# Kernel tuning notes

Hardware: AMD Instinct MI355X
Metric: run time of the kernel (lower is better)

## Reference

```python
import jax, jax.numpy as jnp
import numpy as np

F32 = jnp.float32
G_VEC = jnp.array([0.0, 0.0, -9.80665], dtype=F32)
# KITTI-style filter parameters (process / initial covariances)
COV_OMEGA = 1e-3; COV_ACC = 1e-2; COV_B_OMEGA = 6e-9; COV_B_ACC = 2e-4
COV_ROT_C_I = 1e-9; COV_T_C_I = 1e-9
COV_ROT0 = 1e-3; COV_V0 = 1e-1; COV_B_OMEGA0 = 1e-1; COV_B_ACC0 = 1e-1
COV_ROT_C_I0 = 1e-6; COV_T_C_I0 = 1e-5
Q_DIAG = jnp.array([COV_OMEGA]*3 + [COV_ACC]*3 + [COV_B_OMEGA]*3 + [COV_B_ACC]*3
                   + [COV_ROT_C_I]*3 + [COV_T_C_I]*3, dtype=F32)


def skew(x):
    z = jnp.zeros((), x.dtype)
    return jnp.stack([jnp.stack([z, -x[2], x[1]]),
                      jnp.stack([x[2], z, -x[0]]),
                      jnp.stack([-x[1], x[0], z])])


def so3exp(phi):
    I = jnp.eye(3, dtype=phi.dtype)
    angle = jnp.linalg.norm(phi)
    small = angle < 1e-8
    a = jnp.where(small, 1.0, angle)
    S = skew(phi)
    R = I + (jnp.sin(a) / a) * S + ((1.0 - jnp.cos(a)) / (a * a)) * (S @ S)
    return jnp.where(small, I + S, R)


def sen3exp(xi):
    phi = xi[:3]
    I = jnp.eye(3, dtype=xi.dtype)
    angle = jnp.linalg.norm(phi)
    small = angle < 1e-8
    a = jnp.where(small, 1.0, angle)
    S = skew(phi)
    SS = S @ S
    Rot = jnp.where(small, I + S,
                    I + (jnp.sin(a) / a) * S + ((1.0 - jnp.cos(a)) / (a * a)) * SS)
    J = jnp.where(small, I + 0.5 * S,
                  I + ((1.0 - jnp.cos(a)) / (a * a)) * S + ((a - jnp.sin(a)) / (a ** 3)) * SS)
    x = J @ xi[3:9].reshape(2, 3).T  # (3,2): columns dv, dp
    return Rot, x


def from_rpy(roll, pitch, yaw):
    c, s = jnp.cos, jnp.sin
    z = jnp.zeros((), roll.dtype); o = jnp.ones((), roll.dtype)
    Rz = jnp.stack([jnp.stack([c(yaw), -s(yaw), z]), jnp.stack([s(yaw), c(yaw), z]), jnp.stack([z, z, o])])
    Ry = jnp.stack([jnp.stack([c(pitch), z, s(pitch)]), jnp.stack([z, o, z]), jnp.stack([-s(pitch), z, c(pitch)])])
    Rx = jnp.stack([jnp.stack([o, z, z]), jnp.stack([z, c(roll), -s(roll)]), jnp.stack([z, s(roll), c(roll)])])
    return Rz @ Ry @ Rx


def _run(t, u, measurements_covs, v_mes, ang0, w_init):
    I3 = jnp.eye(3, dtype=F32)
    IdP = jnp.eye(21, dtype=F32)
    Q = jnp.diag(Q_DIAG)
    dt = t[1:] - t[:-1]
    # InitProcessCovNet.init_cov: beta = 10 ** tanh(W @ 1)
    beta = 10.0 ** jnp.tanh(w_init)
    P0 = jnp.zeros((21, 21), F32)
    I2 = jnp.eye(2, dtype=F32)
    P0 = P0.at[:2, :2].set(COV_ROT0 * beta[0] * I2)
    P0 = P0.at[3:5, 3:5].set(COV_V0 * beta[1] * I2)
    P0 = P0.at[9:12, 9:12].set(COV_B_OMEGA0 * beta[2] * I3)
    P0 = P0.at[12:15, 12:15].set(COV_B_ACC0 * beta[3] * I3)
    P0 = P0.at[15:18, 15:18].set(COV_ROT_C_I0 * beta[4] * I3)
    P0 = P0.at[18:21, 18:21].set(COV_T_C_I0 * beta[5] * I3)
    Rot0 = from_rpy(ang0[0], ang0[1], ang0[2])
    z3 = jnp.zeros(3, F32)
    state0 = (Rot0, v_mes[0], z3, z3, z3, I3, z3, P0)

    def step(carry, inp):
        Rot_p, v_p, p_p, bo_p, ba_p, Rci_p, tci_p, P = carry
        u_i, dt_i, mc_i = inp
        # ---- propagate ----
        acc = Rot_p @ (u_i[3:6] - ba_p) + G_VEC
        v = v_p + acc * dt_i
        p = p_p + v_p * dt_i + 0.5 * acc * dt_i * dt_i
        omega = (u_i[:3] - bo_p) * dt_i
        Rot = Rot_p @ so3exp(omega)
        # ---- covariance propagation ----
        vsr = skew(v_p) @ Rot_p
        psr = skew(p_p) @ Rot_p
        F = jnp.zeros((21, 21), F32)
        F = F.at[3:6, :3].set(skew(G_VEC))
        F = F.at[6:9, 3:6].set(I3)
        F = F.at[3:6, 12:15].set(-Rot_p)
        F = F.at[:3, 9:12].set(-Rot_p)
        F = F.at[3:6, 9:12].set(-vsr)
        F = F.at[6:9, 9:12].set(-psr)
        Gm = jnp.zeros((21, 18), F32)
        Gm = Gm.at[:3, :3].set(Rot_p)
        Gm = Gm.at[3:6, 3:6].set(Rot_p)
        Gm = Gm.at[3:6, :3].set(vsr)
        Gm = Gm.at[6:9, :3].set(psr)
        Gm = Gm.at[9:12, 6:9].set(I3)
        Gm = Gm.at[12:15, 9:12].set(I3)
        Gm = Gm.at[15:18, 12:15].set(I3)
        Gm = Gm.at[18:21, 15:18].set(I3)
        F = F * dt_i
        Gm = Gm * dt_i
        F2 = F @ F
        Phi = IdP + F + 0.5 * F2 + (F2 @ F) / 6.0
        P = Phi @ (P + Gm @ Q @ Gm.T) @ Phi.T
        # ---- update (zero lateral/vertical body velocity pseudo-measurement) ----
        Rot_body = Rot @ Rci_p
        v_imu = Rot.T @ v
        om = u_i[:3] - bo_p
        v_body = Rci_p.T @ v_imu + skew(tci_p) @ om
        Omega = skew(om)
        H_v_imu = Rci_p.T @ skew(v_imu)
        H_t = skew(tci_p)
        H = jnp.zeros((2, 21), F32)
        H = H.at[:, 3:6].set(Rot_body.T[1:])
        H = H.at[:, 15:18].set(H_v_imu[1:])
        H = H.at[:, 9:12].set(H_t[1:])
        H = H.at[:, 18:21].set(-Omega[1:])
        r = -v_body[1:]
        Rm = jnp.diag(mc_i)
        S = H @ P @ H.T + Rm
        K = jnp.linalg.solve(S, (P @ H.T).T).T  # (21,2)
        dx = K @ r
        dR, dxi = sen3exp(dx[:9])
        Rot_u = dR @ Rot
        v_u = dR @ v + dxi[:, 0]
        p_u = dR @ p + dxi[:, 1]
        bo_u = bo_p + dx[9:12]
        ba_u = ba_p + dx[12:15]
        Rci_u = so3exp(dx[15:18]) @ Rci_p
        tci_u = tci_p + dx[18:21]
        I_KH = IdP - K @ H
        P_u = I_KH @ P @ I_KH.T + K @ Rm @ K.T
        P_u = 0.5 * (P_u + P_u.T)
        new = (Rot_u, v_u, p_u, bo_u, ba_u, Rci_u, tci_u, P_u)
        return new, (Rot_u, v_u, p_u, bo_u, ba_u, Rci_u, tci_u)

    xs = (u[1:], dt, measurements_covs[1:])
    _, traj = jax.lax.scan(step, state0, xs)
    cat = lambda x0, xs_: jnp.concatenate([x0[None], xs_], axis=0)
    Rot = cat(Rot0, traj[0]); v = cat(state0[1], traj[1]); p = cat(state0[2], traj[2])
    bo = cat(state0[3], traj[3]); ba = cat(state0[4], traj[4])
    Rci = cat(I3, traj[5]); tci = cat(state0[6], traj[6])
    n = Rot.shape[0]
    # pack (Rot, v, p, b_omega, b_acc, Rot_c_i, t_c_i) -> [N, 30]
    return jnp.concatenate([Rot.reshape(n, 9), v, p, bo, ba, Rci.reshape(n, 9), tci], axis=1)


def setup_inputs() -> dict:
    key = jax.random.key(0)
    k1, k2, k3, k4, k5, k6 = jax.random.split(key, 6)
    N = 5000
    t = jnp.arange(N, dtype=F32) * 0.01  # 100 Hz IMU timestamps
    u = 0.1 * jax.random.normal(k1, (N, 6), dtype=F32)
    u = u.at[:, 5].add(9.80665)  # accel z ~ gravity
    measurements_covs = 0.5 * jax.random.uniform(k2, (N, 2), dtype=F32) + 0.1
    v_mes = jax.random.normal(k3, (N, 3), dtype=F32)
    p_mes = jax.random.normal(k4, (N, 3), dtype=F32)
    ang0 = 0.1 * jax.random.normal(k5, (3,), dtype=F32)
    w_init = 0.1 * jax.random.normal(k6, (6,), dtype=F32)
    return {"t": t, "u": u, "measurements_covs": measurements_covs,
            "v_mes": v_mes, "p_mes": p_mes, "ang0": ang0, "w_init": w_init, "N": N}


def reference(t, u, measurements_covs, v_mes, p_mes, ang0, w_init, N):
    # p_mes is accepted (as in run()) but unused: p[0] stays zero in init_run.
    return _run(t, u, measurements_covs, v_mes, ang0, w_init)
```

## Files before the change

kernel.cpp:

```cpp
#include <hip/hip_runtime.h>
#include <math.h>

#define GRV 9.80665f

__device__ __forceinline__ void so3coeffs(float a2, float* c1, float* c2, float* c3){
  if (a2 < 2.5e-3f){
    float a4 = a2*a2;
    *c1 = 1.f      - a2*(1.f/6.f)   + a4*(1.f/120.f);
    *c2 = 0.5f     - a2*(1.f/24.f)  + a4*(1.f/720.f);
    *c3 = (1.f/6.f)- a2*(1.f/120.f) + a4*(1.f/5040.f);
  } else {
    float a = sqrtf(a2);
    float sa = sinf(a), ca = cosf(a);
    *c1 = sa/a; *c2 = (1.f-ca)/a2; *c3 = (a-sa)/(a2*a);
  }
}

__device__ __forceinline__ void so3exp_u(float p0, float p1, float p2, float* R){
  float a2 = p0*p0+p1*p1+p2*p2;
  float c1,c2,c3; so3coeffs(a2,&c1,&c2,&c3);
  R[0]=1.f+c2*(p0*p0-a2); R[4]=1.f+c2*(p1*p1-a2); R[8]=1.f+c2*(p2*p2-a2);
  R[1]=-c1*p2+c2*p0*p1;   R[3]= c1*p2+c2*p0*p1;
  R[2]= c1*p1+c2*p0*p2;   R[6]=-c1*p1+c2*p0*p2;
  R[5]=-c1*p0+c2*p1*p2;   R[7]= c1*p0+c2*p1*p2;
}

__device__ __forceinline__ void mat3mul_u(const float* A, const float* B, float* C){
  #pragma unroll
  for (int r=0;r<3;r++)
    #pragma unroll
    for (int c=0;c<3;c++)
      C[r*3+c] = A[r*3]*B[c] + A[r*3+1]*B[3+c] + A[r*3+2]*B[6+c];
}

__device__ __forceinline__ void col_update(float* a, const float* R_, const float* n13,
                                           const float* n23, float dtv, float hdt2,
                                           float Gdt, float Ghdt2){
  float nb[9];
  #pragma unroll
  for (int jb=0;jb<3;jb++)
    nb[jb] = a[jb] - dtv*(R_[jb*3]*a[9]+R_[jb*3+1]*a[10]+R_[jb*3+2]*a[11]);
  #pragma unroll
  for (int r=0;r<3;r++){
    float s = a[3+r];
    if (r==0) s += Gdt*a[1];
    if (r==1) s -= Gdt*a[0];
    s += n13[r*3]*a[9]+n13[r*3+1]*a[10]+n13[r*3+2]*a[11];
    s -= dtv*(R_[r*3]*a[12]+R_[r*3+1]*a[13]+R_[r*3+2]*a[14]);
    nb[3+r]=s;
  }
  #pragma unroll
  for (int r=0;r<3;r++){
    float s = a[6+r];
    if (r==0) s += Ghdt2*a[1];
    if (r==1) s -= Ghdt2*a[0];
    s += dtv*a[3+r];
    s += n23[r*3]*a[9]+n23[r*3+1]*a[10]+n23[r*3+2]*a[11];
    s -= hdt2*(R_[r*3]*a[12]+R_[r*3+1]*a[13]+R_[r*3+2]*a[14]);
    nb[6+r]=s;
  }
  #pragma unroll
  for (int k=0;k<9;k++) a[k]=nb[k];
}

__global__ __launch_bounds__(64)
void iekf_kernel(const float* __restrict__ t, const float* __restrict__ u,
                 const float* __restrict__ mcov, const float* __restrict__ vmes,
                 const float* __restrict__ ang0, const float* __restrict__ winit,
                 float* __restrict__ out, int N)
{
  const int lane = threadIdx.x;
  const int cl   = (lane<21)? lane : 20;

  __shared__ float TP1[21*24];
  __shared__ float TP2[21*24];
  __shared__ float PH[44];
  __shared__ float stG[36];

  float R_[9], v_[3], p_[3], bo_[3], ba_[3], Rci_[9], tci_[3];
  float creg[21];

  float beta[6];
  #pragma unroll
  for (int k=0;k<6;k++) beta[k] = powf(10.f, tanhf(winit[k]));
  {
    float cr=cosf(ang0[0]), sr=sinf(ang0[0]);
    float cp=cosf(ang0[1]), sp=sinf(ang0[1]);
    float cy=cosf(ang0[2]), sy=sinf(ang0[2]);
    float Rz[9]={cy,-sy,0.f, sy,cy,0.f, 0.f,0.f,1.f};
    float Ry[9]={cp,0.f,sp, 0.f,1.f,0.f, -sp,0.f,cp};
    float Rx[9]={1.f,0.f,0.f, 0.f,cr,-sr, 0.f,sr,cr};
    float T1m[9]; mat3mul_u(Rz,Ry,T1m); mat3mul_u(T1m,Rx,R_);
  }
  v_[0]=vmes[0]; v_[1]=vmes[1]; v_[2]=vmes[2];
  #pragma unroll
  for (int k=0;k<3;k++){ p_[k]=0.f; bo_[k]=0.f; ba_[k]=0.f; tci_[k]=0.f; }
  #pragma unroll
  for (int k=0;k<9;k++) Rci_[k] = (k%4==0)?1.f:0.f;

  {
    float dl = (lane==0||lane==1)? 1e-3f*beta[0]
             : (lane==3||lane==4)? 0.1f*beta[1]
             : (lane>=9&&lane<12)? 0.1f*beta[2]
             : (lane>=12&&lane<15)? 0.1f*beta[3]
             : (lane>=15&&lane<18)? 1e-6f*beta[4]
             : (lane>=18&&lane<21)? 1e-5f*beta[5] : 0.f;
    #pragma unroll
    for (int j=0;j<21;j++) creg[j] = (j==lane)? dl : 0.f;
  }

  if (lane==0){
    ((float4*)stG)[0] = make_float4(R_[0],R_[1],R_[2],R_[3]);
    ((float4*)stG)[1] = make_float4(R_[4],R_[5],R_[6],R_[7]);
    ((float4*)stG)[2] = make_float4(R_[8],v_[0],v_[1],v_[2]);
    ((float4*)stG)[3] = make_float4(p_[0],p_[1],p_[2],bo_[0]);
    ((float4*)stG)[4] = make_float4(bo_[1],bo_[2],ba_[0],ba_[1]);
    ((float4*)stG)[5] = make_float4(ba_[2],Rci_[0],Rci_[1],Rci_[2]);
    ((float4*)stG)[6] = make_float4(Rci_[3],Rci_[4],Rci_[5],Rci_[6]);
    ((float4*)stG)[7] = make_float4(Rci_[7],Rci_[8],tci_[0],tci_[1]);
    ((float4*)stG)[8] = make_float4(tci_[2],0.f,0.f,0.f);
  }

  float t_nm1 = t[0];
  float t_n   = (N>1)? t[1] : t[0];
  float mc0   = (N>1)? mcov[2] : 0.f;
  float mc1   = (N>1)? mcov[3] : 0.f;
  float u6[6] = {0,0,0,0,0,0};
  if (N>1){
    #pragma unroll
    for (int k=0;k<6;k++) u6[k]=u[6+k];
  }

  for (int n=1; n<N; n++){
    const float dtv = t_n - t_nm1;
    const float dt2 = dtv*dtv;
    const float hdt2 = 0.5f*dt2;
    const float sdt3 = dt2*dtv*(1.f/6.f);
    const float Gdt = GRV*dtv;
    const float Ghdt2 = GRV*hdt2;

    if (lane<33) out[(size_t)(n-1)*33 + lane] = stG[lane];

    if (lane<21){
      float4* rp = (float4*)&TP1[lane*24];
      rp[0]=make_float4(creg[0],creg[1],creg[2],creg[3]);
      rp[1]=make_float4(creg[4],creg[5],creg[6],creg[7]);
      rp[2]=make_float4(creg[8],creg[9],creg[10],creg[11]);
      rp[3]=make_float4(creg[12],creg[13],creg[14],creg[15]);
      rp[4]=make_float4(creg[16],creg[17],creg[18],creg[19]);
      TP1[lane*24+20]=creg[20];
    }
    float colv[21];
    #pragma unroll
    for (int r=0;r<21;r++) colv[r] = TP1[r*24+cl];

    float vsr[9], psr[9], n13[9], n23[9];
    #pragma unroll
    for (int c=0;c<3;c++){
      vsr[c]   = v_[1]*R_[6+c] - v_[2]*R_[3+c];
      vsr[3+c] = v_[2]*R_[c]   - v_[0]*R_[6+c];
      vsr[6+c] = v_[0]*R_[3+c] - v_[1]*R_[c];
      psr[c]   = p_[1]*R_[6+c] - p_[2]*R_[3+c];
      psr[3+c] = p_[2]*R_[c]   - p_[0]*R_[6+c];
      psr[6+c] = p_[0]*R_[3+c] - p_[1]*R_[c];
    }
    #pragma unroll
    for (int c=0;c<3;c++){
      float sg0 =  GRV*R_[3+c];
      float sg1 = -GRV*R_[c];
      n13[c]   = -dtv*vsr[c]   - hdt2*sg0;
      n13[3+c] = -dtv*vsr[3+c] - hdt2*sg1;
      n13[6+c] = -dtv*vsr[6+c];
      n23[c]   = -dtv*psr[c]   - hdt2*vsr[c]   - sdt3*sg0;
      n23[3+c] = -dtv*psr[3+c] - hdt2*vsr[3+c] - sdt3*sg1;
      n23[6+c] = -dtv*psr[6+c] - hdt2*vsr[6+c];
    }
    const float vv = v_[0]*v_[0]+v_[1]*v_[1]+v_[2]*v_[2];
    const float vp = v_[0]*p_[0]+v_[1]*p_[1]+v_[2]*p_[2];
    const float pp = p_[0]*p_[0]+p_[1]*p_[1]+p_[2]*p_[2];

    float areg[21];
    #pragma unroll
    for (int j=0;j<21;j++) areg[j] = 0.5f*(creg[j] + colv[j]);
    {
      const float qom = 1e-3f*dt2, qac = 1e-2f*dt2;
      if (lane<9){
        int bi = lane/3, r3 = lane - 3*bi;
        float vrr = (r3==0)?v_[0]:(r3==1)?v_[1]:v_[2];
        float prr = (r3==0)?p_[0]:(r3==1)?p_[1]:p_[2];
        float sv0 = (r3==0)?0.f:(r3==1)? v_[2]:-v_[1];
        float sv1 = (r3==0)?-v_[2]:(r3==1)?0.f: v_[0];
        float sv2 = (r3==0)? v_[1]:(r3==1)?-v_[0]:0.f;
        float sp0 = (r3==0)?0.f:(r3==1)? p_[2]:-p_[1];
        float sp1 = (r3==0)?-p_[2]:(r3==1)?0.f: p_[0];
        float sp2 = (r3==0)? p_[1]:(r3==1)?-p_[0]:0.f;
        if (bi==0){
          areg[r3]  += qom;
          areg[3] -= qom*sv0; areg[4] -= qom*sv1; areg[5] -= qom*sv2;
          areg[6] -= qom*sp0; areg[7] -= qom*sp1; areg[8] -= qom*sp2;
        } else if (bi==1){
          areg[0] += qom*sv0; areg[1] += qom*sv1; areg[2] += qom*sv2;
          areg[3+r3] += qom*vv + qac;
          areg[3] -= qom*vrr*v_[0]; areg[4] -= qom*vrr*v_[1]; areg[5] -= qom*vrr*v_[2];
          areg[6+r3] += qom*vp;
          areg[6] -= qom*prr*v_[0]; areg[7] -= qom*prr*v_[1]; areg[8] -= qom*prr*v_[2];
        } else {
          areg[0] += qom*sp0; areg[1] += qom*sp1; areg[2] += qom*sp2;
          areg[3+r3] += qom*vp;
          areg[3] -= qom*vrr*p_[0]; areg[4] -= qom*vrr*p_[1]; areg[5] -= qom*vrr*p_[2];
          areg[6+r3] += qom*pp;
          areg[6] -= qom*prr*p_[0]; areg[7] -= qom*prr*p_[1]; areg[8] -= qom*prr*p_[2];
        }
      }
      #pragma unroll
      for (int j=9;j<21;j++){
        float qd = (j<12)? 6e-9f : (j<15)? 2e-4f : 1e-9f;
        areg[j] += (lane==j)? qd*dt2 : 0.f;
      }
    }

    col_update(areg, R_, n13, n23, dtv, hdt2, Gdt, Ghdt2);

    if (lane<21){
      float4* rp = (float4*)&TP2[lane*24];
      rp[0]=make_float4(areg[0],areg[1],areg[2],areg[3]);
      rp[1]=make_float4(areg[4],areg[5],areg[6],areg[7]);
      rp[2]=make_float4(areg[8],areg[9],areg[10],areg[11]);
      rp[3]=make_float4(areg[12],areg[13],areg[14],areg[15]);
      rp[4]=make_float4(areg[16],areg[17],areg[18],areg[19]);
      TP2[lane*24+20]=areg[20];
    }
    float ctreg[21];
    #pragma unroll
    for (int r=0;r<21;r++) ctreg[r] = TP2[r*24+cl];

    float Rn[9], vnp[3], pnp[3];
    {
      float ub0=u6[3]-ba_[0], ub1=u6[4]-ba_[1], ub2=u6[5]-ba_[2];
      float ac0=R_[0]*ub0+R_[1]*ub1+R_[2]*ub2;
      float ac1=R_[3]*ub0+R_[4]*ub1+R_[5]*ub2;
      float ac2=R_[6]*ub0+R_[7]*ub1+R_[8]*ub2 - GRV;
      vnp[0]=v_[0]+ac0*dtv; vnp[1]=v_[1]+ac1*dtv; vnp[2]=v_[2]+ac2*dtv;
      pnp[0]=p_[0]+v_[0]*dtv+0.5f*ac0*dt2;
      pnp[1]=p_[1]+v_[1]*dtv+0.5f*ac1*dt2;
      pnp[2]=p_[2]+v_[2]*dtv+0.5f*ac2*dt2;
      float E[9]; so3exp_u((u6[0]-bo_[0])*dtv,(u6[1]-bo_[1])*dtv,(u6[2]-bo_[2])*dtv, E);
      mat3mul_u(R_, E, Rn);
    }
    float h0_3,h0_4,h0_5,h0_9,h0_11,h0_15,h0_16,h0_17,h0_18,h0_20;
    float h1_3,h1_4,h1_5,h1_9,h1_10,h1_15,h1_16,h1_17,h1_18,h1_19;
    float rsh0, rsh1;
    {
      float Rb[9]; mat3mul_u(Rn, Rci_, Rb);
      float vi0 = Rn[0]*vnp[0]+Rn[3]*vnp[1]+Rn[6]*vnp[2];
      float vi1 = Rn[1]*vnp[0]+Rn[4]*vnp[1]+Rn[7]*vnp[2];
      float vi2 = Rn[2]*vnp[0]+Rn[5]*vnp[1]+Rn[8]*vnp[2];
      float o0 = u6[0]-bo_[0], o1 = u6[1]-bo_[1], o2 = u6[2]-bo_[2];
      h0_3 = Rb[1]; h0_4 = Rb[4]; h0_5 = Rb[7];
      h1_3 = Rb[2]; h1_4 = Rb[5]; h1_5 = Rb[8];
      h0_9 = tci_[2];  h0_11 = -tci_[0];
      h1_9 = -tci_[1]; h1_10 = tci_[0];
      h0_15 =  Rci_[4]*vi2 - Rci_[7]*vi1;
      h0_16 = -Rci_[1]*vi2 + Rci_[7]*vi0;
      h0_17 =  Rci_[1]*vi1 - Rci_[4]*vi0;
      h1_15 =  Rci_[5]*vi2 - Rci_[8]*vi1;
      h1_16 = -Rci_[2]*vi2 + Rci_[8]*vi0;
      h1_17 =  Rci_[2]*vi1 - Rci_[5]*vi0;
      h0_18 = -o2; h0_20 = o0;
      h1_18 =  o1; h1_19 = -o0;
      rsh0 = -( Rci_[1]*vi0 + Rci_[4]*vi1 + Rci_[7]*vi2 + (tci_[2]*o0 - tci_[0]*o2) );
      rsh1 = -( Rci_[2]*vi0 + Rci_[5]*vi1 + Rci_[8]*vi2 + (-tci_[1]*o0 + tci_[0]*o1) );
    }

    col_update(ctreg, R_, n13, n23, dtv, hdt2, Gdt, Ghdt2);

    float ph0 = (((ctreg[3]*h0_3 + ctreg[4]*h0_4) + (ctreg[5]*h0_5 + ctreg[9]*h0_9)) +
                 ((ctreg[11]*h0_11 + ctreg[15]*h0_15) + (ctreg[16]*h0_16 + ctreg[17]*h0_17))) +
                (ctreg[18]*h0_18 + ctreg[20]*h0_20);
    float ph1 = (((ctreg[3]*h1_3 + ctreg[4]*h1_4) + (ctreg[5]*h1_5 + ctreg[9]*h1_9)) +
                 ((ctreg[10]*h1_10 + ctreg[15]*h1_15) + (ctreg[16]*h1_16 + ctreg[17]*h1_17))) +
                (ctreg[18]*h1_18 + ctreg[19]*h1_19);
    if (lane<21) *(float2*)&PH[lane*2] = make_float2(ph0, ph1);

    float pj0[21], pj1[21];
    {
      #pragma unroll
      for (int q=0;q<11;q++){
        float4 v4 = ((float4*)PH)[q];
        if (2*q   < 21){ pj0[2*q]   = v4.x; pj1[2*q]   = v4.y; }
        if (2*q+1 < 21){ pj0[2*q+1] = v4.z; pj1[2*q+1] = v4.w; }
      }
    }

    float s00 = mc0 + ((((h0_3*pj0[3] + h0_4*pj0[4]) + (h0_5*pj0[5] + h0_9*pj0[9])) +
                        ((h0_11*pj0[11] + h0_15*pj0[15]) + (h0_16*pj0[16] + h0_17*pj0[17]))) +
                       (h0_18*pj0[18] + h0_20*pj0[20]));
    float s01 =        ((((h0_3*pj1[3] + h0_4*pj1[4]) + (h0_5*pj1[5] + h0_9*pj1[9])) +
                        ((h0_11*pj1[11] + h0_15*pj1[15]) + (h0_16*pj1[16] + h0_17*pj1[17]))) +
                       (h0_18*pj1[18] + h0_20*pj1[20]));
    float s10 =        ((((h1_3*pj0[3] + h1_4*pj0[4]) + (h1_5*pj0[5] + h1_9*pj0[9])) +
                        ((h1_10*pj0[10] + h1_15*pj0[15]) + (h1_16*pj0[16] + h1_17*pj0[17]))) +
                       (h1_18*pj0[18] + h1_19*pj0[19]));
    float s11 = mc1 + ((((h1_3*pj1[3] + h1_4*pj1[4]) + (h1_5*pj1[5] + h1_9*pj1[9])) +
                        ((h1_10*pj1[10] + h1_15*pj1[15]) + (h1_16*pj1[16] + h1_17*pj1[17]))) +
                       (h1_18*pj1[18] + h1_19*pj1[19]));
    float id  = 1.f/(s00*s11 - s01*s10);
    float i00 =  s11*id, i01 = -s01*id, i10 = -s10*id, i11 = s00*id;
    float sm01 = 0.5f*(s01+s10);
    float g0 = i00*rsh0 + i01*rsh1;
    float g1 = i10*rsh0 + i11*rsh1;

    float dx[21];
    #pragma unroll
    for (int j=0;j<21;j++) dx[j] = pj0[j]*g0 + pj1[j]*g1;

    {
      float ki0 = ph0*i00 + ph1*i10;
      float ki1 = ph0*i01 + ph1*i11;
      float ai0 = s00*ki0 + sm01*ki1;
      float ai1 = sm01*ki0 + s11*ki1;
      float al = -ki0 + (ai0 - ph0)*i00 + (ai1 - ph1)*i01;
      float be = -ki1 + (ai0 - ph0)*i10 + (ai1 - ph1)*i11;
      #pragma unroll
      for (int j=0;j<21;j++) creg[j] = ctreg[j] + al*pj0[j] + be*pj1[j];
    }

    {
      float q0=dx[0], q1=dx[1], q2=dx[2];
      float a2 = q0*q0+q1*q1+q2*q2;
      float c1,c2,c3; so3coeffs(a2,&c1,&c2,&c3);
      float dR[9], Jm[9];
      dR[0]=1.f+c2*(q0*q0-a2); dR[4]=1.f+c2*(q1*q1-a2); dR[8]=1.f+c2*(q2*q2-a2);
      dR[1]=-c1*q2+c2*q0*q1;   dR[3]= c1*q2+c2*q0*q1;
      dR[2]= c1*q1+c2*q0*q2;   dR[6]=-c1*q1+c2*q0*q2;
      dR[5]=-c1*q0+c2*q1*q2;   dR[7]= c1*q0+c2*q1*q2;
      Jm[0]=1.f+c3*(q0*q0-a2); Jm[4]=1.f+c3*(q1*q1-a2); Jm[8]=1.f+c3*(q2*q2-a2);
      Jm[1]=-c2*q2+c3*q0*q1;   Jm[3]= c2*q2+c3*q0*q1;
      Jm[2]= c2*q1+c3*q0*q2;   Jm[6]=-c2*q1+c3*q0*q2;
      Jm[5]=-c2*q0+c3*q1*q2;   Jm[7]= c2*q0+c3*q1*q2;
      float xv[3], xp[3];
      #pragma unroll
      for (int r=0;r<3;r++){
        xv[r]=Jm[r*3]*dx[3]+Jm[r*3+1]*dx[4]+Jm[r*3+2]*dx[5];
        xp[r]=Jm[r*3]*dx[6]+Jm[r*3+1]*dx[7]+Jm[r*3+2]*dx[8];
      }
      float Rn2[9]; mat3mul_u(dR, Rn, Rn2);
      #pragma unroll
      for (int r=0;r<3;r++){
        float vv2 = dR[r*3]*vnp[0]+dR[r*3+1]*vnp[1]+dR[r*3+2]*vnp[2] + xv[r];
        float pp2 = dR[r*3]*pnp[0]+dR[r*3+1]*pnp[1]+dR[r*3+2]*pnp[2] + xp[r];
        v_[r]=vv2; p_[r]=pp2;
        bo_[r]+=dx[9+r]; ba_[r]+=dx[12+r]; tci_[r]+=dx[18+r];
      }
      float E2[9]; so3exp_u(dx[15],dx[16],dx[17],E2);
      float Rc2[9]; mat3mul_u(E2, Rci_, Rc2);
      #pragma unroll
      for (int k=0;k<9;k++){ Rci_[k]=Rc2[k]; R_[k]=Rn2[k]; }
    }
    if (lane==0){
      ((float4*)stG)[0] = make_float4(R_[0],R_[1],R_[2],R_[3]);
      ((float4*)stG)[1] = make_float4(R_[4],R_[5],R_[6],R_[7]);
      ((float4*)stG)[2] = make_float4(R_[8],v_[0],v_[1],v_[2]);
      ((float4*)stG)[3] = make_float4(p_[0],p_[1],p_[2],bo_[0]);
      ((float4*)stG)[4] = make_float4(bo_[1],bo_[2],ba_[0],ba_[1]);
      ((float4*)stG)[5] = make_float4(ba_[2],Rci_[0],Rci_[1],Rci_[2]);
      ((float4*)stG)[6] = make_float4(Rci_[3],Rci_[4],Rci_[5],Rci_[6]);
      ((float4*)stG)[7] = make_float4(Rci_[7],Rci_[8],tci_[0],tci_[1]);
      ((float4*)stG)[8] = make_float4(tci_[2],0.f,0.f,0.f);
    }

    {
      int np = n+1;
      t_nm1 = t_n;
      if (np < N){
        t_n = t[np];
        mc0 = mcov[np*2]; mc1 = mcov[np*2+1];
        #pragma unroll
        for (int k=0;k<6;k++) u6[k]=u[np*6+k];
      }
    }
  }

  if (lane<33) out[(size_t)(N-1)*33 + lane] = stG[lane];
}

extern "C" void kernel_launch(void* const* d_in, const int* in_sizes, int n_in,
                              void* d_out, int out_size, void* d_ws, size_t ws_size,
                              hipStream_t stream) {
  const float* t     = (const float*)d_in[0];
  const float* u     = (const float*)d_in[1];
  const float* mcov  = (const float*)d_in[2];
  const float* vmes  = (const float*)d_in[3];
  const float* ang0  = (const float*)d_in[5];
  const float* winit = (const float*)d_in[6];
  float* out = (float*)d_out;
  int N = in_sizes[0];
  iekf_kernel<<<dim3(1), dim3(64), 0, stream>>>(t, u, mcov, vmes, ang0, winit, out, N);
}
```

Measured before the change: 15.94 ms.

## Split IEKF step across two wavefronts for covariance and state paths

Launches 128 threads and gives the covariance propagation (the two col_update passes and transposes) to wave 0, while wave 1 does state propagation, the measurement Jacobian, the state correction and the output stores. Values pass between the waves through shared memory (state, H, PH), with three block barriers per step. The aim is to run the independent state and covariance work at the same time on one CU instead of serially in a single wave. In exchange it adds barrier and LDS round-trip latency to every step of a strictly sequential loop.

```diff
diff --git a/kernel.cpp b/kernel.cpp
--- a/kernel.cpp
+++ b/kernel.cpp
@@ -63,26 +63,23 @@
   for (int k=0;k<9;k++) a[k]=nb[k];
 }
 
-__global__ __launch_bounds__(64)
+__global__ __launch_bounds__(128)
 void iekf_kernel(const float* __restrict__ t, const float* __restrict__ u,
                  const float* __restrict__ mcov, const float* __restrict__ vmes,
                  const float* __restrict__ ang0, const float* __restrict__ winit,
                  float* __restrict__ out, int N)
 {
-  const int lane = threadIdx.x;
-  const int cl   = (lane<21)? lane : 20;
-
-  __shared__ float TP1[21*24];
-  __shared__ float TP2[21*24];
-  __shared__ float PH[44];
-  __shared__ float stG[36];
+  const int tid  = threadIdx.x;
+  const int lane = tid & 63;
+  const bool w0  = (tid < 64);
+
+  __shared__ float TP[21*24];
+  __shared__ float stS[36];
+  __shared__ float Hb[20];
+  __shared__ float PHb[44];
 
   float R_[9], v_[3], p_[3], bo_[3], ba_[3], Rci_[9], tci_[3];
-  float creg[21];
-
-  float beta[6];
-  #pragma unroll
-  for (int k=0;k<6;k++) beta[k] = powf(10.f, tanhf(winit[k]));
+
   {
     float cr=cosf(ang0[0]), sr=sinf(ang0[0]);
     float cp=cosf(ang0[1]), sp=sinf(ang0[1]);
@@ -98,7 +95,25 @@
   #pragma unroll
   for (int k=0;k<9;k++) Rci_[k] = (k%4==0)?1.f:0.f;
 
-  {
+  if (tid==0){
+    ((float4*)stS)[0] = make_float4(R_[0],R_[1],R_[2],R_[3]);
+    ((float4*)stS)[1] = make_float4(R_[4],R_[5],R_[6],R_[7]);
+    ((float4*)stS)[2] = make_float4(R_[8],v_[0],v_[1],v_[2]);
+    ((float4*)stS)[3] = make_float4(p_[0],p_[1],p_[2],bo_[0]);
+    ((float4*)stS)[4] = make_float4(bo_[1],bo_[2],ba_[0],ba_[1]);
+    ((float4*)stS)[5] = make_float4(ba_[2],Rci_[0],Rci_[1],Rci_[2]);
+    ((float4*)stS)[6] = make_float4(Rci_[3],Rci_[4],Rci_[5],Rci_[6]);
+    ((float4*)stS)[7] = make_float4(Rci_[7],Rci_[8],tci_[0],tci_[1]);
+    ((float4*)stS)[8] = make_float4(tci_[2],0.f,0.f,0.f);
+  }
+
+  float creg[21], colv[21];
+  #pragma unroll
+  for (int j=0;j<21;j++){ creg[j]=0.f; colv[j]=0.f; }
+  if (w0){
+    float beta[6];
+    #pragma unroll
+    for (int k=0;k<6;k++) beta[k] = powf(10.f, tanhf(winit[k]));
     float dl = (lane==0||lane==1)? 1e-3f*beta[0]
              : (lane==3||lane==4)? 0.1f*beta[1]
              : (lane>=9&&lane<12)? 0.1f*beta[2]
@@ -107,18 +122,14 @@
              : (lane>=18&&lane<21)? 1e-5f*beta[5] : 0.f;
     #pragma unroll
     for (int j=0;j<21;j++) creg[j] = (j==lane)? dl : 0.f;
-  }
-
-  if (lane==0){
-    ((float4*)stG)[0] = make_float4(R_[0],R_[1],R_[2],R_[3]);
-    ((float4*)stG)[1] = make_float4(R_[4],R_[5],R_[6],R_[7]);
-    ((float4*)stG)[2] = make_float4(R_[8],v_[0],v_[1],v_[2]);
-    ((float4*)stG)[3] = make_float4(p_[0],p_[1],p_[2],bo_[0]);
-    ((float4*)stG)[4] = make_float4(bo_[1],bo_[2],ba_[0],ba_[1]);
-    ((float4*)stG)[5] = make_float4(ba_[2],Rci_[0],Rci_[1],Rci_[2]);
-    ((float4*)stG)[6] = make_float4(Rci_[3],Rci_[4],Rci_[5],Rci_[6]);
-    ((float4*)stG)[7] = make_float4(Rci_[7],Rci_[8],tci_[0],tci_[1]);
-    ((float4*)stG)[8] = make_float4(tci_[2],0.f,0.f,0.f);
+    if (lane<21){
+      #pragma unroll
+      for (int j=0;j<21;j++) TP[j*24+lane]=creg[j];
+    }
+    if (lane<21){
+      #pragma unroll
+      for (int j=0;j<21;j++) colv[j]=TP[lane*24+j];
+    }
   }
 
   float t_nm1 = t[0];
@@ -126,195 +137,209 @@
   float mc0   = (N>1)? mcov[2] : 0.f;
   float mc1   = (N>1)? mcov[3] : 0.f;
   float u6[6] = {0,0,0,0,0,0};
-  if (N>1){
+  if (!w0 && N>1){
     #pragma unroll
     for (int k=0;k<6;k++) u6[k]=u[6+k];
   }
 
+  __syncthreads();
+
+  float h03=0,h04=0,h05=0,h09=0,h011=0,h015=0,h016=0,h017=0,h018=0,h020=0;
+  float h13=0,h14=0,h15=0,h19=0,h110=0,h115=0,h116=0,h117=0,h118=0,h119=0;
+  float rsh0=0, rsh1=0;
+  float Rn[9], vnp[3], pnp[3];
+  float ctreg[21];
+  float ph0=0.f, ph1=0.f;
+
   for (int n=1; n<N; n++){
-    const float dtv = t_n - t_nm1;
-    const float dt2 = dtv*dtv;
+    const float dtv  = t_n - t_nm1;
+    const float dt2  = dtv*dtv;
     const float hdt2 = 0.5f*dt2;
     const float sdt3 = dt2*dtv*(1.f/6.f);
-    const float Gdt = GRV*dtv;
-    const float Ghdt2 = GRV*hdt2;
-
-    if (lane<33) out[(size_t)(n-1)*33 + lane] = stG[lane];
-
-    if (lane<21){
-      float4* rp = (float4*)&TP1[lane*24];
-      rp[0]=make_float4(creg[0],creg[1],creg[2],creg[3]);
-      rp[1]=make_float4(creg[4],creg[5],creg[6],creg[7]);
-      rp[2]=make_float4(creg[8],creg[9],creg[10],creg[11]);
-      rp[3]=make_float4(creg[12],creg[13],creg[14],creg[15]);
-      rp[4]=make_float4(creg[16],creg[17],creg[18],creg[19]);
-      TP1[lane*24+20]=creg[20];
-    }
-    float colv[21];
-    #pragma unroll
-    for (int r=0;r<21;r++) colv[r] = TP1[r*24+cl];
-
-    float vsr[9], psr[9], n13[9], n23[9];
-    #pragma unroll
-    for (int c=0;c<3;c++){
-      vsr[c]   = v_[1]*R_[6+c] - v_[2]*R_[3+c];
-      vsr[3+c] = v_[2]*R_[c]   - v_[0]*R_[6+c];
-      vsr[6+c] = v_[0]*R_[3+c] - v_[1]*R_[c];
-      psr[c]   = p_[1]*R_[6+c] - p_[2]*R_[3+c];
-      psr[3+c] = p_[2]*R_[c]   - p_[0]*R_[6+c];
-      psr[6+c] = p_[0]*R_[3+c] - p_[1]*R_[c];
-    }
-    #pragma unroll
-    for (int c=0;c<3;c++){
-      float sg0 =  GRV*R_[3+c];
-      float sg1 = -GRV*R_[c];
-      n13[c]   = -dtv*vsr[c]   - hdt2*sg0;
-      n13[3+c] = -dtv*vsr[3+c] - hdt2*sg1;
-      n13[6+c] = -dtv*vsr[6+c];
-      n23[c]   = -dtv*psr[c]   - hdt2*vsr[c]   - sdt3*sg0;
-      n23[3+c] = -dtv*psr[3+c] - hdt2*vsr[3+c] - sdt3*sg1;
-      n23[6+c] = -dtv*psr[6+c] - hdt2*vsr[6+c];
-    }
-    const float vv = v_[0]*v_[0]+v_[1]*v_[1]+v_[2]*v_[2];
-    const float vp = v_[0]*p_[0]+v_[1]*p_[1]+v_[2]*p_[2];
-    const float pp = p_[0]*p_[0]+p_[1]*p_[1]+p_[2]*p_[2];
-
-    float areg[21];
-    #pragma unroll
-    for (int j=0;j<21;j++) areg[j] = 0.5f*(creg[j] + colv[j]);
-    {
-      const float qom = 1e-3f*dt2, qac = 1e-2f*dt2;
-      if (lane<9){
-        int bi = lane/3, r3 = lane - 3*bi;
-        float vrr = (r3==0)?v_[0]:(r3==1)?v_[1]:v_[2];
-        float prr = (r3==0)?p_[0]:(r3==1)?p_[1]:p_[2];
-        float sv0 = (r3==0)?0.f:(r3==1)? v_[2]:-v_[1];
-        float sv1 = (r3==0)?-v_[2]:(r3==1)?0.f: v_[0];
-        float sv2 = (r3==0)? v_[1]:(r3==1)?-v_[0]:0.f;
-        float sp0 = (r3==0)?0.f:(r3==1)? p_[2]:-p_[1];
-        float sp1 = (r3==0)?-p_[2]:(r3==1)?0.f: p_[0];
-        float sp2 = (r3==0)? p_[1]:(r3==1)?-p_[0]:0.f;
-        if (bi==0){
-          areg[r3]  += qom;
-          areg[3] -= qom*sv0; areg[4] -= qom*sv1; areg[5] -= qom*sv2;
-          areg[6] -= qom*sp0; areg[7] -= qom*sp1; areg[8] -= qom*sp2;
-        } else if (bi==1){
-          areg[0] += qom*sv0; areg[1] += qom*sv1; areg[2] += qom*sv2;
-          areg[3+r3] += qom*vv + qac;
-          areg[3] -= qom*vrr*v_[0]; areg[4] -= qom*vrr*v_[1]; areg[5] -= qom*vrr*v_[2];
-          areg[6+r3] += qom*vp;
-          areg[6] -= qom*prr*v_[0]; areg[7] -= qom*prr*v_[1]; areg[8] -= qom*prr*v_[2];
-        } else {
-          areg[0] += qom*sp0; areg[1] += qom*sp1; areg[2] += qom*sp2;
-          areg[3+r3] += qom*vp;
-          areg[3] -= qom*vrr*p_[0]; areg[4] -= qom*vrr*p_[1]; areg[5] -= qom*vrr*p_[2];
-          areg[6+r3] += qom*pp;
-          areg[6] -= qom*prr*p_[0]; areg[7] -= qom*prr*p_[1]; areg[8] -= qom*prr*p_[2];
+    const float Gdt  = GRV*dtv;
+    const float Ghdt2= GRV*hdt2;
+
+    if (w0){
+      {
+        float4 s0=((float4*)stS)[0], s1=((float4*)stS)[1], s2=((float4*)stS)[2], s3=((float4*)stS)[3];
+        R_[0]=s0.x; R_[1]=s0.y; R_[2]=s0.z; R_[3]=s0.w;
+        R_[4]=s1.x; R_[5]=s1.y; R_[6]=s1.z; R_[7]=s1.w;
+        R_[8]=s2.x; v_[0]=s2.y; v_[1]=s2.z; v_[2]=s2.w;
+        p_[0]=s3.x; p_[1]=s3.y; p_[2]=s3.z;
+      }
+      float vsr[9], psr[9], n13[9], n23[9];
+      #pragma unroll
+      for (int c=0;c<3;c++){
+        vsr[c]   = v_[1]*R_[6+c] - v_[2]*R_[3+c];
+        vsr[3+c] = v_[2]*R_[c]   - v_[0]*R_[6+c];
+        vsr[6+c] = v_[0]*R_[3+c] - v_[1]*R_[c];
+        psr[c]   = p_[1]*R_[6+c] - p_[2]*R_[3+c];
+        psr[3+c] = p_[2]*R_[c]   - p_[0]*R_[6+c];
+        psr[6+c] = p_[0]*R_[3+c] - p_[1]*R_[c];
+      }
+      #pragma unroll
+      for (int c=0;c<3;c++){
+        float sg0 =  GRV*R_[3+c];
+        float sg1 = -GRV*R_[c];
+        n13[c]   = -dtv*vsr[c]   - hdt2*sg0;
+        n13[3+c] = -dtv*vsr[3+c] - hdt2*sg1;
+        n13[6+c] = -dtv*vsr[6+c];
+        n23[c]   = -dtv*psr[c]   - hdt2*vsr[c]   - sdt3*sg0;
+        n23[3+c] = -dtv*psr[3+c] - hdt2*vsr[3+c] - sdt3*sg1;
+        n23[6+c] = -dtv*psr[6+c] - hdt2*vsr[6+c];
+      }
+      const float vv = v_[0]*v_[0]+v_[1]*v_[1]+v_[2]*v_[2];
+      const float vp = v_[0]*p_[0]+v_[1]*p_[1]+v_[2]*p_[2];
+      const float pp = p_[0]*p_[0]+p_[1]*p_[1]+p_[2]*p_[2];
+
+      float areg[21];
+      #pragma unroll
+      for (int j=0;j<21;j++) areg[j] = 0.5f*(creg[j] + colv[j]);
+      {
+        const float qom = 1e-3f*dt2, qac = 1e-2f*dt2;
+        if (lane<9){
+          int bi = lane/3, r3 = lane - 3*bi;
+          float vrr = (r3==0)?v_[0]:(r3==1)?v_[1]:v_[2];
+          float prr = (r3==0)?p_[0]:(r3==1)?p_[1]:p_[2];
+          float sv0 = (r3==0)?0.f:(r3==1)? v_[2]:-v_[1];
+          float sv1 = (r3==0)?-v_[2]:(r3==1)?0.f: v_[0];
+          float sv2 = (r3==0)? v_[1]:(r3==1)?-v_[0]:0.f;
+          float sp0 = (r3==0)?0.f:(r3==1)? p_[2]:-p_[1];
+          float sp1 = (r3==0)?-p_[2]:(r3==1)?0.f: p_[0];
+          float sp2 = (r3==0)? p_[1]:(r3==1)?-p_[0]:0.f;
+          if (bi==0){
+            areg[r3]  += qom;
+            areg[3] -= qom*sv0; areg[4] -= qom*sv1; areg[5] -= qom*sv2;
+            areg[6] -= qom*sp0; areg[7] -= qom*sp1; areg[8] -= qom*sp2;
+          } else if (bi==1){
+            areg[0] += qom*sv0; areg[1] += qom*sv1; areg[2] += qom*sv2;
+            areg[3+r3] += qom*vv + qac;
+            areg[3] -= qom*vrr*v_[0]; areg[4] -= qom*vrr*v_[1]; areg[5] -= qom*vrr*v_[2];
+            areg[6+r3] += qom*vp;
+            areg[6] -= qom*prr*v_[0]; areg[7] -= qom*prr*v_[1]; areg[8] -= qom*prr*v_[2];
+          } else {
+            areg[0] += qom*sp0; areg[1] += qom*sp1; areg[2] += qom*sp2;
+            areg[3+r3] += qom*vp;
+            areg[3] -= qom*vrr*p_[0]; areg[4] -= qom*vrr*p_[1]; areg[5] -= qom*vrr*p_[2];
+            areg[6+r3] += qom*pp;
+            areg[6] -= qom*prr*p_[0]; areg[7] -= qom*prr*p_[1]; areg[8] -= qom*prr*p_[2];
+          }
         }
-      }
-      #pragma unroll
-      for (int j=9;j<21;j++){
-        float qd = (j<12)? 6e-9f : (j<15)? 2e-4f : 1e-9f;
-        areg[j] += (lane==j)? qd*dt2 : 0.f;
-      }
-    }
-
-    col_update(areg, R_, n13, n23, dtv, hdt2, Gdt, Ghdt2);
-
-    if (lane<21){
-      float4* rp = (float4*)&TP2[lane*24];
-      rp[0]=make_float4(areg[0],areg[1],areg[2],areg[3]);
-      rp[1]=make_float4(areg[4],areg[5],areg[6],areg[7]);
-      rp[2]=make_float4(areg[8],areg[9],areg[10],areg[11]);
-      rp[3]=make_float4(areg[12],areg[13],areg[14],areg[15]);
-      rp[4]=make_float4(areg[16],areg[17],areg[18],areg[19]);
-      TP2[lane*24+20]=areg[20];
-    }
-    float ctreg[21];
-    #pragma unroll
-    for (int r=0;r<21;r++) ctreg[r] = TP2[r*24+cl];
-
-    float Rn[9], vnp[3], pnp[3];
-    {
-      float ub0=u6[3]-ba_[0], ub1=u6[4]-ba_[1], ub2=u6[5]-ba_[2];
-      float ac0=R_[0]*ub0+R_[1]*ub1+R_[2]*ub2;
-      float ac1=R_[3]*ub0+R_[4]*ub1+R_[5]*ub2;
-      float ac2=R_[6]*ub0+R_[7]*ub1+R_[8]*ub2 - GRV;
-      vnp[0]=v_[0]+ac0*dtv; vnp[1]=v_[1]+ac1*dtv; vnp[2]=v_[2]+ac2*dtv;
-      pnp[0]=p_[0]+v_[0]*dtv+0.5f*ac0*dt2;
-      pnp[1]=p_[1]+v_[1]*dtv+0.5f*ac1*dt2;
-      pnp[2]=p_[2]+v_[2]*dtv+0.5f*ac2*dt2;
-      float E[9]; so3exp_u((u6[0]-bo_[0])*dtv,(u6[1]-bo_[1])*dtv,(u6[2]-bo_[2])*dtv, E);
-      mat3mul_u(R_, E, Rn);
-    }
-    float h0_3,h0_4,h0_5,h0_9,h0_11,h0_15,h0_16,h0_17,h0_18,h0_20;
-    float h1_3,h1_4,h1_5,h1_9,h1_10,h1_15,h1_16,h1_17,h1_18,h1_19;
-    float rsh0, rsh1;
-    {
-      float Rb[9]; mat3mul_u(Rn, Rci_, Rb);
-      float vi0 = Rn[0]*vnp[0]+Rn[3]*vnp[1]+Rn[6]*vnp[2];
-      float vi1 = Rn[1]*vnp[0]+Rn[4]*vnp[1]+Rn[7]*vnp[2];
-      float vi2 = Rn[2]*vnp[0]+Rn[5]*vnp[1]+Rn[8]*vnp[2];
-      float o0 = u6[0]-bo_[0], o1 = u6[1]-bo_[1], o2 = u6[2]-bo_[2];
-      h0_3 = Rb[1]; h0_4 = Rb[4]; h0_5 = Rb[7];
-      h1_3 = Rb[2]; h1_4 = Rb[5]; h1_5 = Rb[8];
-      h0_9 = tci_[2];  h0_11 = -tci_[0];
-      h1_9 = -tci_[1]; h1_10 = tci_[0];
-      h0_15 =  Rci_[4]*vi2 - Rci_[7]*vi1;
-      h0_16 = -Rci_[1]*vi2 + Rci_[7]*vi0;
-      h0_17 =  Rci_[1]*vi1 - Rci_[4]*vi0;
-      h1_15 =  Rci_[5]*vi2 - Rci_[8]*vi1;
-      h1_16 = -Rci_[2]*vi2 + Rci_[8]*vi0;
-      h1_17 =  Rci_[2]*vi1 - Rci_[5]*vi0;
-      h0_18 = -o2; h0_20 = o0;
-      h1_18 =  o1; h1_19 = -o0;
-      rsh0 = -( Rci_[1]*vi0 + Rci_[4]*vi1 + Rci_[7]*vi2 + (tci_[2]*o0 - tci_[0]*o2) );
-      rsh1 = -( Rci_[2]*vi0 + Rci_[5]*vi1 + Rci_[8]*vi2 + (-tci_[1]*o0 + tci_[0]*o1) );
-    }
-
-    col_update(ctreg, R_, n13, n23, dtv, hdt2, Gdt, Ghdt2);
-
-    float ph0 = (((ctreg[3]*h0_3 + ctreg[4]*h0_4) + (ctreg[5]*h0_5 + ctreg[9]*h0_9)) +
-                 ((ctreg[11]*h0_11 + ctreg[15]*h0_15) + (ctreg[16]*h0_16 + ctreg[17]*h0_17))) +
-                (ctreg[18]*h0_18 + ctreg[20]*h0_20);
-    float ph1 = (((ctreg[3]*h1_3 + ctreg[4]*h1_4) + (ctreg[5]*h1_5 + ctreg[9]*h1_9)) +
-                 ((ctreg[10]*h1_10 + ctreg[15]*h1_15) + (ctreg[16]*h1_16 + ctreg[17]*h1_17))) +
-                (ctreg[18]*h1_18 + ctreg[19]*h1_19);
-    if (lane<21) *(float2*)&PH[lane*2] = make_float2(ph0, ph1);
+        #pragma unroll
+        for (int j=9;j<21;j++){
+          float qd = (j<12)? 6e-9f : (j<15)? 2e-4f : 1e-9f;
+          areg[j] += (lane==j)? qd*dt2 : 0.f;
+        }
+      }
+      if (lane>=21){
+        #pragma unroll
+        for (int j=0;j<21;j++) areg[j]=0.f;
+      }
+
+      col_update(areg, R_, n13, n23, dtv, hdt2, Gdt, Ghdt2);
+
+      if (lane<21){
+        #pragma unroll
+        for (int j=0;j<21;j++) TP[j*24+lane]=areg[j];
+      }
+      if (lane<21){
+        #pragma unroll
+        for (int j=0;j<21;j++) ctreg[j]=TP[lane*24+j];
+      } else {
+        #pragma unroll
+        for (int j=0;j<21;j++) ctreg[j]=0.f;
+      }
+
+      col_update(ctreg, R_, n13, n23, dtv, hdt2, Gdt, Ghdt2);
+    } else {
+      if (lane<33) out[(size_t)(n-1)*33 + lane] = stS[lane];
+      {
+        float ub0=u6[3]-ba_[0], ub1=u6[4]-ba_[1], ub2=u6[5]-ba_[2];
+        float ac0=R_[0]*ub0+R_[1]*ub1+R_[2]*ub2;
+        float ac1=R_[3]*ub0+R_[4]*ub1+R_[5]*ub2;
+        float ac2=R_[6]*ub0+R_[7]*ub1+R_[8]*ub2 - GRV;
+        vnp[0]=v_[0]+ac0*dtv; vnp[1]=v_[1]+ac1*dtv; vnp[2]=v_[2]+ac2*dtv;
+        pnp[0]=p_[0]+v_[0]*dtv+0.5f*ac0*dt2;
+        pnp[1]=p_[1]+v_[1]*dtv+0.5f*ac1*dt2;
+        pnp[2]=p_[2]+v_[2]*dtv+0.5f*ac2*dt2;
+        float E[9]; so3exp_u((u6[0]-bo_[0])*dtv,(u6[1]-bo_[1])*dtv,(u6[2]-bo_[2])*dtv, E);
+        mat3mul_u(R_, E, Rn);
+      }
+      {
+        float Rb[9]; mat3mul_u(Rn, Rci_, Rb);
+        float vi0 = Rn[0]*vnp[0]+Rn[3]*vnp[1]+Rn[6]*vnp[2];
+        float vi1 = Rn[1]*vnp[0]+Rn[4]*vnp[1]+Rn[7]*vnp[2];
+        float vi2 = Rn[2]*vnp[0]+Rn[5]*vnp[1]+Rn[8]*vnp[2];
+        float o0 = u6[0]-bo_[0], o1 = u6[1]-bo_[1], o2 = u6[2]-bo_[2];
+        h03 = Rb[1]; h04 = Rb[4]; h05 = Rb[7];
+        h13 = Rb[2]; h14 = Rb[5]; h15 = Rb[8];
+        h09 = tci_[2];  h011 = -tci_[0];
+        h19 = -tci_[1]; h110 = tci_[0];
+        h015 =  Rci_[4]*vi2 - Rci_[7]*vi1;
+        h016 = -Rci_[1]*vi2 + Rci_[7]*vi0;
+        h017 =  Rci_[1]*vi1 - Rci_[4]*vi0;
+        h115 =  Rci_[5]*vi2 - Rci_[8]*vi1;
+        h116 = -Rci_[2]*vi2 + Rci_[8]*vi0;
+        h117 =  Rci_[2]*vi1 - Rci_[5]*vi0;
+        h018 = -o2; h020 = o0;
+        h118 =  o1; h119 = -o0;
+        rsh0 = -( Rci_[1]*vi0 + Rci_[4]*vi1 + Rci_[7]*vi2 + (tci_[2]*o0 - tci_[0]*o2) );
+        rsh1 = -( Rci_[2]*vi0 + Rci_[5]*vi1 + Rci_[8]*vi2 + (-tci_[1]*o0 + tci_[0]*o1) );
+      }
+      if (lane==0){
+        ((float4*)Hb)[0] = make_float4(h03,h04,h05,h09);
+        ((float4*)Hb)[1] = make_float4(h011,h015,h016,h017);
+        ((float4*)Hb)[2] = make_float4(h018,h020,h13,h14);
+        ((float4*)Hb)[3] = make_float4(h15,h19,h110,h115);
+        ((float4*)Hb)[4] = make_float4(h116,h117,h118,h119);
+      }
+    }
+    __syncthreads();
+
+    if (w0){
+      float4 b0=((float4*)Hb)[0], b1=((float4*)Hb)[1], b2=((float4*)Hb)[2];
+      float4 b3=((float4*)Hb)[3], b4=((float4*)Hb)[4];
+      h03=b0.x; h04=b0.y; h05=b0.z; h09=b0.w;
+      h011=b1.x; h015=b1.y; h016=b1.z; h017=b1.w;
+      h018=b2.x; h020=b2.y; h13=b2.z; h14=b2.w;
+      h15=b3.x; h19=b3.y; h110=b3.z; h115=b3.w;
+      h116=b4.x; h117=b4.y; h118=b4.z; h119=b4.w;
+      ph0 = (((ctreg[3]*h03 + ctreg[4]*h04) + (ctreg[5]*h05 + ctreg[9]*h09)) +
+             ((ctreg[11]*h011 + ctreg[15]*h015) + (ctreg[16]*h016 + ctreg[17]*h017))) +
+            (ctreg[18]*h018 + ctreg[20]*h020);
+      ph1 = (((ctreg[3]*h13 + ctreg[4]*h14) + (ctreg[5]*h15 + ctreg[9]*h19)) +
+             ((ctreg[10]*h110 + ctreg[15]*h115) + (ctreg[16]*h116 + ctreg[17]*h117))) +
+            (ctreg[18]*h118 + ctreg[19]*h119);
+      if (lane<21) *(float2*)&PHb[lane*2] = make_float2(ph0, ph1);
+    }
+    __syncthreads();
 
     float pj0[21], pj1[21];
     {
       #pragma unroll
       for (int q=0;q<11;q++){
-        float4 v4 = ((float4*)PH)[q];
+        float4 v4 = ((float4*)PHb)[q];
         if (2*q   < 21){ pj0[2*q]   = v4.x; pj1[2*q]   = v4.y; }
         if (2*q+1 < 21){ pj0[2*q+1] = v4.z; pj1[2*q+1] = v4.w; }
       }
     }
-
-    float s00 = mc0 + ((((h0_3*pj0[3] + h0_4*pj0[4]) + (h0_5*pj0[5] + h0_9*pj0[9])) +
-                        ((h0_11*pj0[11] + h0_15*pj0[15]) + (h0_16*pj0[16] + h0_17*pj0[17]))) +
-                       (h0_18*pj0[18] + h0_20*pj0[20]));
-    float s01 =        ((((h0_3*pj1[3] + h0_4*pj1[4]) + (h0_5*pj1[5] + h0_9*pj1[9])) +
-                        ((h0_11*pj1[11] + h0_15*pj1[15]) + (h0_16*pj1[16] + h0_17*pj1[17]))) +
-                       (h0_18*pj1[18] + h0_20*pj1[20]));
-    float s10 =        ((((h1_3*pj0[3] + h1_4*pj0[4]) + (h1_5*pj0[5] + h1_9*pj0[9])) +
-                        ((h1_10*pj0[10] + h1_15*pj0[15]) + (h1_16*pj0[16] + h1_17*pj0[17]))) +
-                       (h1_18*pj0[18] + h1_19*pj0[19]));
-    float s11 = mc1 + ((((h1_3*pj1[3] + h1_4*pj1[4]) + (h1_5*pj1[5] + h1_9*pj1[9])) +
-                        ((h1_10*pj1[10] + h1_15*pj1[15]) + (h1_16*pj1[16] + h1_17*pj1[17]))) +
-                       (h1_18*pj1[18] + h1_19*pj1[19]));
+    float s00 = mc0 + ((((h03*pj0[3] + h04*pj0[4]) + (h05*pj0[5] + h09*pj0[9])) +
+                        ((h011*pj0[11] + h015*pj0[15]) + (h016*pj0[16] + h017*pj0[17]))) +
+                       (h018*pj0[18] + h020*pj0[20]));
+    float s01 =        ((((h03*pj1[3] + h04*pj1[4]) + (h05*pj1[5] + h09*pj1[9])) +
+                        ((h011*pj1[11] + h015*pj1[15]) + (h016*pj1[16] + h017*pj1[17]))) +
+                       (h018*pj1[18] + h020*pj1[20]));
+    float s10 =        ((((h13*pj0[3] + h14*pj0[4]) + (h15*pj0[5] + h19*pj0[9])) +
+                        ((h110*pj0[10] + h115*pj0[15]) + (h116*pj0[16] + h117*pj0[17]))) +
+                       (h118*pj0[18] + h119*pj0[19]));
+    float s11 = mc1 + ((((h13*pj1[3] + h14*pj1[4]) + (h15*pj1[5] + h19*pj1[9])) +
+                        ((h110*pj1[10] + h115*pj1[15]) + (h116*pj1[16] + h117*pj1[17]))) +
+                       (h118*pj1[18] + h119*pj1[19]));
     float id  = 1.f/(s00*s11 - s01*s10);
     float i00 =  s11*id, i01 = -s01*id, i10 = -s10*id, i11 = s00*id;
     float sm01 = 0.5f*(s01+s10);
-    float g0 = i00*rsh0 + i01*rsh1;
-    float g1 = i10*rsh0 + i11*rsh1;
-
-    float dx[21];
-    #pragma unroll
-    for (int j=0;j<21;j++) dx[j] = pj0[j]*g0 + pj1[j]*g1;
-
-    {
+
+    if (w0){
       float ki0 = ph0*i00 + ph1*i10;
       float ki1 = ph0*i01 + ph1*i11;
       float ai0 = s00*ki0 + sm01*ki1;
@@ -323,50 +348,63 @@
       float be = -ki1 + (ai0 - ph0)*i10 + (ai1 - ph1)*i11;
       #pragma unroll
       for (int j=0;j<21;j++) creg[j] = ctreg[j] + al*pj0[j] + be*pj1[j];
-    }
-
-    {
-      float q0=dx[0], q1=dx[1], q2=dx[2];
-      float a2 = q0*q0+q1*q1+q2*q2;
-      float c1,c2,c3; so3coeffs(a2,&c1,&c2,&c3);
-      float dR[9], Jm[9];
-      dR[0]=1.f+c2*(q0*q0-a2); dR[4]=1.f+c2*(q1*q1-a2); dR[8]=1.f+c2*(q2*q2-a2);
-      dR[1]=-c1*q2+c2*q0*q1;   dR[3]= c1*q2+c2*q0*q1;
-      dR[2]= c1*q1+c2*q0*q2;   dR[6]=-c1*q1+c2*q0*q2;
-      dR[5]=-c1*q0+c2*q1*q2;   dR[7]= c1*q0+c2*q1*q2;
-      Jm[0]=1.f+c3*(q0*q0-a2); Jm[4]=1.f+c3*(q1*q1-a2); Jm[8]=1.f+c3*(q2*q2-a2);
-      Jm[1]=-c2*q2+c3*q0*q1;   Jm[3]= c2*q2+c3*q0*q1;
-      Jm[2]= c2*q1+c3*q0*q2;   Jm[6]=-c2*q1+c3*q0*q2;
-      Jm[5]=-c2*q0+c3*q1*q2;   Jm[7]= c2*q0+c3*q1*q2;
-      float xv[3], xp[3];
-      #pragma unroll
-      for (int r=0;r<3;r++){
-        xv[r]=Jm[r*3]*dx[3]+Jm[r*3+1]*dx[4]+Jm[r*3+2]*dx[5];
-        xp[r]=Jm[r*3]*dx[6]+Jm[r*3+1]*dx[7]+Jm[r*3+2]*dx[8];
-      }
-      float Rn2[9]; mat3mul_u(dR, Rn, Rn2);
-      #pragma unroll
-      for (int r=0;r<3;r++){
-        float vv2 = dR[r*3]*vnp[0]+dR[r*3+1]*vnp[1]+dR[r*3+2]*vnp[2] + xv[r];
-        float pp2 = dR[r*3]*pnp[0]+dR[r*3+1]*pnp[1]+dR[r*3+2]*pnp[2] + xp[r];
-        v_[r]=vv2; p_[r]=pp2;
-        bo_[r]+=dx[9+r]; ba_[r]+=dx[12+r]; tci_[r]+=dx[18+r];
-      }
-      float E2[9]; so3exp_u(dx[15],dx[16],dx[17],E2);
-      float Rc2[9]; mat3mul_u(E2, Rci_, Rc2);
-      #pragma unroll
-      for (int k=0;k<9;k++){ Rci_[k]=Rc2[k]; R_[k]=Rn2[k]; }
-    }
-    if (lane==0){
-      ((float4*)stG)[0] = make_float4(R_[0],R_[1],R_[2],R_[3]);
-      ((float4*)stG)[1] = make_float4(R_[4],R_[5],R_[6],R_[7]);
-      ((float4*)stG)[2] = make_float4(R_[8],v_[0],v_[1],v_[2]);
-      ((float4*)stG)[3] = make_float4(p_[0],p_[1],p_[2],bo_[0]);
-      ((float4*)stG)[4] = make_float4(bo_[1],bo_[2],ba_[0],ba_[1]);
-      ((float4*)stG)[5] = make_float4(ba_[2],Rci_[0],Rci_[1],Rci_[2]);
-      ((float4*)stG)[6] = make_float4(Rci_[3],Rci_[4],Rci_[5],Rci_[6]);
-      ((float4*)stG)[7] = make_float4(Rci_[7],Rci_[8],tci_[0],tci_[1]);
-      ((float4*)stG)[8] = make_float4(tci_[2],0.f,0.f,0.f);
+      if (lane<21){
+        #pragma unroll
+        for (int j=0;j<21;j++) TP[j*24+lane]=creg[j];
+      }
+      if (lane<21){
+        #pragma unroll
+        for (int j=0;j<21;j++) colv[j]=TP[lane*24+j];
+      }
+    } else {
+      float g0 = i00*rsh0 + i01*rsh1;
+      float g1 = i10*rsh0 + i11*rsh1;
+      float dx[21];
+      #pragma unroll
+      for (int j=0;j<21;j++) dx[j] = pj0[j]*g0 + pj1[j]*g1;
+      {
+        float q0=dx[0], q1=dx[1], q2=dx[2];
+        float a2 = q0*q0+q1*q1+q2*q2;
+        float c1,c2,c3; so3coeffs(a2,&c1,&c2,&c3);
+        float dR[9], Jm[9];
+        dR[0]=1.f+c2*(q0*q0-a2); dR[4]=1.f+c2*(q1*q1-a2); dR[8]=1.f+c2*(q2*q2-a2);
+        dR[1]=-c1*q2+c2*q0*q1;   dR[3]= c1*q2+c2*q0*q1;
+        dR[2]= c1*q1+c2*q0*q2;   dR[6]=-c1*q1+c2*q0*q2;
+        dR[5]=-c1*q0+c2*q1*q2;   dR[7]= c1*q0+c2*q1*q2;
+        Jm[0]=1.f+c3*(q0*q0-a2); Jm[4]=1.f+c3*(q1*q1-a2); Jm[8]=1.f+c3*(q2*q2-a2);
+        Jm[1]=-c2*q2+c3*q0*q1;   Jm[3]= c2*q2+c3*q0*q1;
+        Jm[2]= c2*q1+c3*q0*q2;   Jm[6]=-c2*q1+c3*q0*q2;
+        Jm[5]=-c2*q0+c3*q1*q2;   Jm[7]= c2*q0+c3*q1*q2;
+        float xv[3], xp[3];
+        #pragma unroll
+        for (int r=0;r<3;r++){
+          xv[r]=Jm[r*3]*dx[3]+Jm[r*3+1]*dx[4]+Jm[r*3+2]*dx[5];
+          xp[r]=Jm[r*3]*dx[6]+Jm[r*3+1]*dx[7]+Jm[r*3+2]*dx[8];
+        }
+        float Rn2[9]; mat3mul_u(dR, Rn, Rn2);
+        #pragma unroll
+        for (int r=0;r<3;r++){
+          float vv2 = dR[r*3]*vnp[0]+dR[r*3+1]*vnp[1]+dR[r*3+2]*vnp[2] + xv[r];
+          float pp2 = dR[r*3]*pnp[0]+dR[r*3+1]*pnp[1]+dR[r*3+2]*pnp[2] + xp[r];
+          v_[r]=vv2; p_[r]=pp2;
+          bo_[r]+=dx[9+r]; ba_[r]+=dx[12+r]; tci_[r]+=dx[18+r];
+        }
+        float E2[9]; so3exp_u(dx[15],dx[16],dx[17],E2);
+        float Rc2[9]; mat3mul_u(E2, Rci_, Rc2);
+        #pragma unroll
+        for (int k=0;k<9;k++){ Rci_[k]=Rc2[k]; R_[k]=Rn2[k]; }
+      }
+      if (lane==0){
+        ((float4*)stS)[0] = make_float4(R_[0],R_[1],R_[2],R_[3]);
+        ((float4*)stS)[1] = make_float4(R_[4],R_[5],R_[6],R_[7]);
+        ((float4*)stS)[2] = make_float4(R_[8],v_[0],v_[1],v_[2]);
+        ((float4*)stS)[3] = make_float4(p_[0],p_[1],p_[2],bo_[0]);
+        ((float4*)stS)[4] = make_float4(bo_[1],bo_[2],ba_[0],ba_[1]);
+        ((float4*)stS)[5] = make_float4(ba_[2],Rci_[0],Rci_[1],Rci_[2]);
+        ((float4*)stS)[6] = make_float4(Rci_[3],Rci_[4],Rci_[5],Rci_[6]);
+        ((float4*)stS)[7] = make_float4(Rci_[7],Rci_[8],tci_[0],tci_[1]);
+        ((float4*)stS)[8] = make_float4(tci_[2],0.f,0.f,0.f);
+      }
     }
 
     {
@@ -375,13 +413,16 @@
       if (np < N){
         t_n = t[np];
         mc0 = mcov[np*2]; mc1 = mcov[np*2+1];
-        #pragma unroll
-        for (int k=0;k<6;k++) u6[k]=u[np*6+k];
-      }
-    }
-  }
-
-  if (lane<33) out[(size_t)(N-1)*33 + lane] = stG[lane];
+        if (!w0){
+          #pragma unroll
+          for (int k=0;k<6;k++) u6[k]=u[np*6+k];
+        }
+      }
+    }
+    __syncthreads();
+  }
+
+  if (!w0 && lane<33) out[(size_t)(N-1)*33 + lane] = stS[lane];
 }
 
 extern "C" void kernel_launch(void* const* d_in, const int* in_sizes, int n_in,
@@ -395,5 +436,5 @@
   const float* winit = (const float*)d_in[6];
   float* out = (float*)d_out;
   int N = in_sizes[0];
-  iekf_kernel<<<dim3(1), dim3(64), 0, stream>>>(t, u, mcov, vmes, ang0, winit, out, N);
-}
+  iekf_kernel<<<dim3(1), dim3(128), 0, stream>>>(t, u, mcov, vmes, ang0, winit, out, N);
+}
```

After: 14.25 ms. 10.6% less time.
